# Kernel tuning notes

Measured on AMD Instinct MI355X. Metric: run time of the kernel, lower is better.

Reference implementation:

```python
import jax, jax.numpy as jnp
import numpy as np

THETA = 0.7
KS = 3          # deformable-conv kernel size
N = KS * KS     # 9 sampling points


def setup_inputs() -> dict:
    key = jax.random.key(0)
    k = jax.random.split(key, 7)
    B, C, H, W = 2, 256, 64, 64
    x = jax.random.normal(k[0], (B, C, H, W), jnp.float32)
    # offset-predicting conv (3x3, pad 1), 2*N output channels; small init so offsets are sane
    p_w = jax.random.normal(k[1], (2 * N, C, 3, 3), jnp.float32) * 0.01
    p_b = jax.random.normal(k[2], (2 * N,), jnp.float32) * 0.01
    # modulation conv (3x3, pad 1), N output channels
    m_w = jax.random.normal(k[3], (N, C, 3, 3), jnp.float32) * 0.01
    m_b = jnp.zeros((N,), jnp.float32)
    # final deform conv weight (applied as ks x ks, stride ks over the unfolded map), no bias
    dconv_w = jax.random.normal(k[4], (256, C, KS, KS), jnp.float32) * 0.05
    # central-difference conv raw weight, shape (Cout, Cin, 1, 5), no bias
    cdc_w = jax.random.normal(k[5], (256, C, 1, 5), jnp.float32) * 0.05
    return {"x": x, "p_w": p_w, "p_b": p_b, "m_w": m_w, "m_b": m_b,
            "dconv_w": dconv_w, "cdc_w": cdc_w}


def _conv2d(x, w, pad):
    return jax.lax.conv_general_dilated(
        x, w, window_strides=(1, 1), padding=pad,
        dimension_numbers=("NCHW", "OIHW", "NCHW"))


def deform_conv(x, p_w, p_b, m_w, m_b, dconv_w):
    B, C, H, W = x.shape
    same = [(1, 1), (1, 1)]
    offset = _conv2d(x, p_w, same) + p_b[None, :, None, None]          # [B,2N,H,W]
    m = jax.nn.sigmoid(_conv2d(x, m_w, same) + m_b[None, :, None, None])  # [B,N,H,W]

    xp = jnp.pad(x, ((0, 0), (0, 0), (1, 1), (1, 1)))  # zero padding 1
    Hp, Wp = H + 2, W + 2

    # p = p_0 + p_n + offset  (x = row coord, y = col coord; torch meshgrid 'ij')
    p_n_x = jnp.repeat(jnp.arange(-1, 2, dtype=x.dtype), 3)   # [-1,-1,-1,0,0,0,1,1,1]
    p_n_y = jnp.tile(jnp.arange(-1, 2, dtype=x.dtype), 3)     # [-1,0,1,-1,0,1,-1,0,1]
    rows = jnp.arange(1, H + 1, dtype=x.dtype)                # p_0_x
    cols = jnp.arange(1, W + 1, dtype=x.dtype)                # p_0_y
    px = offset[:, :N] + p_n_x[None, :, None, None] + rows[None, None, :, None]
    py = offset[:, N:] + p_n_y[None, :, None, None] + cols[None, None, None, :]
    px = jnp.transpose(px, (0, 2, 3, 1))  # [B,H,W,N]
    py = jnp.transpose(py, (0, 2, 3, 1))

    # integer corners from UNCLAMPED p (detached), as in the original
    fx = jnp.floor(jax.lax.stop_gradient(px))
    fy = jnp.floor(jax.lax.stop_gradient(py))
    qx0 = jnp.clip(fx, 0, Hp - 1)
    qy0 = jnp.clip(fy, 0, Wp - 1)
    qx1 = jnp.clip(fx + 1, 0, Hp - 1)
    qy1 = jnp.clip(fy + 1, 0, Wp - 1)

    # clamp p before computing bilinear weights (original order)
    pxc = jnp.clip(px, 0, Hp - 1)
    pyc = jnp.clip(py, 0, Wp - 1)
    g_lt = (1 + (qx0 - pxc)) * (1 + (qy0 - pyc))
    g_rb = (1 - (qx1 - pxc)) * (1 - (qy1 - pyc))
    g_lb = (1 + (qx0 - pxc)) * (1 - (qy1 - pyc))
    g_rt = (1 - (qx1 - pxc)) * (1 + (qy0 - pyc))

    xf = xp.reshape(B, C, Hp * Wp)

    def gather(qx, qy):
        idx = (qx.astype(jnp.int32) * Wp + qy.astype(jnp.int32)).reshape(B, 1, -1)
        return jnp.take_along_axis(xf, idx, axis=2).reshape(B, C, H, W, N)

    x_off = (g_lt[:, None] * gather(qx0, qy0)
             + g_rb[:, None] * gather(qx1, qy1)
             + g_lb[:, None] * gather(qx0, qy1)
             + g_rt[:, None] * gather(qx1, qy0))          # [B,C,H,W,N]
    x_off = x_off * jnp.transpose(m, (0, 2, 3, 1))[:, None]  # modulation broadcast over C

    # conv(ksxks, stride ks) over the unfolded map == contraction over the N taps;
    # tap n = 3r + c corresponds to kernel position (r, c)
    w = dconv_w.reshape(dconv_w.shape[0], C, N)
    return jnp.einsum("bchwn,ocn->bohw", x_off, w)


def cdc_conv(x, cdc_w):
    Co, Ci = cdc_w.shape[0], cdc_w.shape[1]
    z = jnp.zeros((Co, Ci, 1), cdc_w.dtype)
    wk = jnp.concatenate(
        [z, cdc_w[:, :, :, 0], z, cdc_w[:, :, :, 1], cdc_w[:, :, :, 2],
         cdc_w[:, :, :, 3], z, cdc_w[:, :, :, 4], z], axis=2
    ).reshape(Co, Ci, 3, 3)
    out_normal = _conv2d(x, wk, [(1, 1), (1, 1)])
    kdiff = cdc_w.sum(axis=(2, 3))[:, :, None, None]
    out_diff = _conv2d(x, kdiff, [(0, 0), (0, 0)])
    return out_normal - THETA * out_diff


def reference(x, p_w, p_b, m_w, m_b, dconv_w, cdc_w):
    out_dc = jax.nn.relu(deform_conv(x, p_w, p_b, m_w, m_b, dconv_w))
    out_cdc = jax.nn.relu(cdc_conv(x, cdc_w))
    return jnp.concatenate([out_dc, out_cdc], axis=1)  # [B,512,H,W]
```

## Files before the change

### kernel.cpp

```cpp
#include <hip/hip_runtime.h>
#include <hip/hip_bf16.h>
#include <math.h>

#define XT_BSTRIDE (66*66*256)
#define THETA_ 0.7f

typedef unsigned short u16;
typedef __attribute__((ext_vector_type(8))) short bf16x8;
typedef __attribute__((ext_vector_type(4))) float f32x4;

#define GLOAD16(gp, lp) __builtin_amdgcn_global_load_lds( \
    (const __attribute__((address_space(1))) unsigned int*)(gp), \
    (__attribute__((address_space(3))) unsigned int*)(lp), 16, 0, 0)

#define WAIT_VMCNT(N) asm volatile("s_waitcnt vmcnt(" #N ")" ::: "memory")

__device__ __forceinline__ void bar_fenced() {
  __builtin_amdgcn_sched_barrier(0);
  __builtin_amdgcn_s_barrier();
  __builtin_amdgcn_sched_barrier(0);
}

__device__ __forceinline__ float bf2f(u16 v) {
  union { unsigned u; float f; } x; x.u = ((unsigned)v) << 16; return x.f;
}
__device__ __forceinline__ u16 f2bf(float f) {
  __hip_bfloat16 h = __float2bfloat16(f);
  return *(u16*)&h;
}

__device__ __forceinline__ size_t swz_idx(int row, int k, int KT) {
  int kt = k >> 6, kc = (k >> 3) & 7, kj = k & 7;
  return (size_t)row * KT + kt * 64 + ((kc ^ (row & 7)) << 3) + kj;
}

__global__ __launch_bounds__(256) void prep(
    const float* __restrict__ x, const float* __restrict__ p_w,
    const float* __restrict__ m_w, const float* __restrict__ dconv_w,
    const float* __restrict__ cdc_w, u16* __restrict__ xTb,
    u16* __restrict__ W1t, u16* __restrict__ Wdt, u16* __restrict__ Wct) {
  int blk = blockIdx.x;
  if (blk < 512) {
    int cg = blk & 3;
    int h  = (blk >> 2) & 63;
    int b  = blk >> 8;
    __shared__ float tile[64][65];
    const float* xp = x + ((size_t)(b * 256 + cg * 64)) * 4096 + h * 64;
#pragma unroll
    for (int j = 0; j < 16; j++) {
      int idx = j * 256 + threadIdx.x;
      int ci = idx >> 6, w = idx & 63;
      tile[ci][w] = xp[(size_t)ci * 4096 + w];
    }
    __syncthreads();
    u16* xo = xTb + (size_t)b * XT_BSTRIDE + ((h + 1) * 66 + 1) * 256 + cg * 64;
#pragma unroll
    for (int j = 0; j < 16; j++) {
      int idx = j * 256 + threadIdx.x;
      int w = idx >> 6, ci = idx & 63;
      xo[(size_t)w * 256 + ci] = f2bf(tile[ci][w]);
    }
    return;
  }
  if (blk < 1032) {
    int i = (blk - 512) * 256 + threadIdx.x;
    if (i >= 133120) return;
    int c = i & 255;
    int j = i >> 8;
    int b = (j >= 260) ? 1 : 0;
    int r = j - b * 260;
    int hp, wp;
    if (r < 66)       { hp = 0;        wp = r; }
    else if (r < 132) { hp = 65;       wp = r - 66; }
    else if (r < 196) { hp = r - 131;  wp = 0; }
    else              { hp = r - 195;  wp = 65; }
    xTb[(size_t)b * XT_BSTRIDE + (hp * 66 + wp) * 256 + c] = 0;
    return;
  }
  int i = (blk - 1032) * 256 + threadIdx.x;
  if (i < 73728) {
    int o = i / 2304, k = i % 2304;
    int kp = k >> 8, c = k & 255;
    float v = 0.f;
    if (o < 18)      v = p_w[((size_t)o * 256 + c) * 9 + kp];
    else if (o < 27) v = m_w[((size_t)(o - 18) * 256 + c) * 9 + kp];
    W1t[swz_idx(o, k, 2304)] = f2bf(v);
    return;
  }
  int j = i - 73728;
  if (j < 589824) {
    int o = j / 2304, k = j % 2304;
    int n = k >> 8, c = k & 255;
    Wdt[swz_idx(o, k, 2304)] = f2bf(dconv_w[((size_t)o * 256 + c) * 9 + n]);
    return;
  }
  int j2 = j - 589824;
  if (j2 < 327680) {
    int o = j2 / 1280, k = j2 % 1280;
    int t = k >> 8, c = k & 255;
    const float* cw = cdc_w + ((size_t)o * 256 + c) * 5;
    float v = cw[t];
    if (t == 2) v -= THETA_ * (cw[0] + cw[1] + cw[2] + cw[3] + cw[4]);
    Wct[swz_idx(o, k, 1280)] = f2bf(v);
  }
}

__global__ __launch_bounds__(256) void gather_Ad(const u16* __restrict__ xTb,
                                                 const float* __restrict__ omp,
                                                 const float* __restrict__ p_b,
                                                 const float* __restrict__ m_b,
                                                 u16* __restrict__ Ad) {
  int gid = blockIdx.x * 256 + threadIdx.x;
  int q = gid & 31;
  int s = gid >> 5;
  int p = s / 9, n = s - p * 9;
  int b = p >> 12;
  int hw = p & 4095;
  int h = hw >> 6, w = hw & 63;

  float offx = p_b[n], offy = p_b[9 + n], mraw = m_b[n];
#pragma unroll
  for (int ks = 0; ks < 4; ks++) {
    const float* base = omp + ks * 221184 + b * 110592;
    offx += base[(size_t)n * 4096 + hw];
    offy += base[(size_t)(9 + n) * 4096 + hw];
    mraw += base[(size_t)(18 + n) * 4096 + hw];
  }
  float px = offx + (float)(h + n / 3);
  float py = offy + (float)(w + n % 3);
  float fx = floorf(px), fy = floorf(py);
  float qx0 = fminf(fmaxf(fx, 0.f), 65.f);
  float qy0 = fminf(fmaxf(fy, 0.f), 65.f);
  float qx1 = fminf(fmaxf(fx + 1.f, 0.f), 65.f);
  float qy1 = fminf(fmaxf(fy + 1.f, 0.f), 65.f);
  float pxc = fminf(fmaxf(px, 0.f), 65.f);
  float pyc = fminf(fmaxf(py, 0.f), 65.f);
  float gx0 = 1.f + (qx0 - pxc);
  float gx1 = 1.f - (qx1 - pxc);
  float gy0 = 1.f + (qy0 - pyc);
  float gy1 = 1.f - (qy1 - pyc);
  float m = 1.f / (1.f + expf(-mraw));
  int i0 = (int)qx0 * 66 + (int)qy0;
  int i1 = (int)qx1 * 66 + (int)qy1;
  int i2 = (int)qx0 * 66 + (int)qy1;
  int i3 = (int)qx1 * 66 + (int)qy0;
  float g0 = gx0 * gy0 * m, g1 = gx1 * gy1 * m;
  float g2 = gx0 * gy1 * m, g3 = gx1 * gy0 * m;

  const u16* xb = xTb + (size_t)b * XT_BSTRIDE + q * 8;
  bf16x8 a0 = *(const bf16x8*)(xb + (size_t)i0 * 256);
  bf16x8 a1 = *(const bf16x8*)(xb + (size_t)i1 * 256);
  bf16x8 a2 = *(const bf16x8*)(xb + (size_t)i2 * 256);
  bf16x8 a3 = *(const bf16x8*)(xb + (size_t)i3 * 256);
  bf16x8 ov;
#pragma unroll
  for (int j = 0; j < 8; j++) {
    float v = g0 * bf2f((u16)a0[j]) + g1 * bf2f((u16)a1[j]) +
              g2 * bf2f((u16)a2[j]) + g3 * bf2f((u16)a3[j]);
    ov[j] = (short)f2bf(v);
  }
  int k = n * 256 + q * 8;
  int kt = k >> 6, kc = (k >> 3) & 7;
  *(bf16x8*)(Ad + (size_t)p * 2304 + kt * 64 + (((kc ^ (p & 7)) << 3))) = ov;
}

template <int KTOT, int MODE>
__device__ __forceinline__ void gemm_body(
    const u16* __restrict__ Asrc, const u16* __restrict__ Bt,
    float* __restrict__ outp, int mt, int nt, u16* As, u16* Bs) {
  const int NKT = KTOT / 64;
  const int OCH0 = (MODE == 1) ? 256 : 0;
  int tid = threadIdx.x;
  int wid = tid >> 6, lane = tid & 63;
  int wr = wid >> 1, wc = wid & 1;
  int pbase = mt * 64;
  int obase = nt * 64;
  int l8 = lane >> 3, l7 = lane & 7;
  int lr = lane & 15, lg = lane >> 4;

  f32x4 acc[2][2];
#pragma unroll
  for (int i = 0; i < 2; i++)
#pragma unroll
    for (int j = 0; j < 2; j++) acc[i][j] = {0.f, 0.f, 0.f, 0.f};

  const int dh1[5] = {0, 1, 1, 1, 2}, dw1[5] = {1, 0, 1, 2, 1};

  auto stage = [&](int kt, u16* Ah, u16* Bh) {
    if (MODE == 0) {
#pragma unroll
      for (int i = 0; i < 2; i++) {
        int r0 = wid * 16 + i * 8;
        const u16* g = Asrc + (size_t)(pbase + r0 + l8) * KTOT + kt * 64 + (l7 << 3);
        GLOAD16(g, &Ah[r0 * 64]);
      }
    } else {
      int t = kt >> 2, c0 = (kt & 3) << 6;
      int dh = dh1[t], dw = dw1[t];
#pragma unroll
      for (int i = 0; i < 2; i++) {
        int r0 = wid * 16 + i * 8;
        int r = r0 + l8;
        int p = pbase + r;
        int b = p >> 12, hw = p & 4095, h = hw >> 6, w = hw & 63;
        int chunk = l7 ^ (r & 7);
        const u16* g = Asrc + (size_t)b * XT_BSTRIDE +
                       ((h + dh) * 66 + (w + dw)) * 256 + c0 + (chunk << 3);
        GLOAD16(g, &Ah[r0 * 64]);
      }
    }
#pragma unroll
    for (int i = 0; i < 2; i++) {
      int o0 = wid * 16 + i * 8;
      const u16* g = Bt + (size_t)(obase + o0 + l8) * KTOT + kt * 64 + (l7 << 3);
      GLOAD16(g, &Bh[o0 * 64]);
    }
  };

  stage(0, As, Bs);

  for (int it = 0; it < NKT; it++) {
    int cur = it & 1;
    u16* Ac = As + cur * 4096;
    u16* Bc = Bs + cur * 4096;

    bar_fenced();
    if (it + 1 < NKT) {
      stage(it + 1, As + (cur ^ 1) * 4096, Bs + (cur ^ 1) * 4096);
      WAIT_VMCNT(4);
    } else {
      WAIT_VMCNT(0);
    }
    bar_fenced();

    bf16x8 av[2][2], bv[2][2];
#pragma unroll
    for (int mf = 0; mf < 2; mf++) {
      int r = wr * 32 + mf * 16 + lr;
#pragma unroll
      for (int ks = 0; ks < 2; ks++) {
        int kc = ks * 4 + lg;
        av[mf][ks] = *(const bf16x8*)&Ac[r * 64 + ((kc ^ (r & 7)) << 3)];
      }
    }
#pragma unroll
    for (int nf = 0; nf < 2; nf++) {
      int o = wc * 32 + nf * 16 + lr;
#pragma unroll
      for (int ks = 0; ks < 2; ks++) {
        int kc = ks * 4 + lg;
        bv[nf][ks] = *(const bf16x8*)&Bc[o * 64 + ((kc ^ (o & 7)) << 3)];
      }
    }
#pragma unroll
    for (int nf = 0; nf < 2; nf++)
#pragma unroll
      for (int mf = 0; mf < 2; mf++)
#pragma unroll
        for (int ks = 0; ks < 2; ks++)
          acc[nf][mf] = __builtin_amdgcn_mfma_f32_16x16x32_bf16(
              bv[nf][ks], av[mf][ks], acc[nf][mf], 0, 0, 0);
  }

#pragma unroll
  for (int nf = 0; nf < 2; nf++)
#pragma unroll
    for (int mf = 0; mf < 2; mf++) {
      int p = pbase + wr * 32 + mf * 16 + lr;
      int hw = p & 4095, b = p >> 12;
      int og = OCH0 + obase + wc * 32 + nf * 16 + lg * 4;
      f32x4 v = acc[nf][mf];
#pragma unroll
      for (int e = 0; e < 4; e++)
        outp[(size_t)(b * 512 + og + e) * 4096 + hw] = fmaxf(v[e], 0.f);
    }
}

__device__ __forceinline__ void offmod_body(
    const u16* __restrict__ xTb, const u16* __restrict__ Bt,
    float* __restrict__ outp, int mt, int kt0, int nkt, u16* As, u16* Bs) {
  int tid = threadIdx.x;
  int wid = tid >> 6, lane = tid & 63;
  int pbase = mt * 128;
  int l8 = lane >> 3, l7 = lane & 7;
  int lr = lane & 15, lg = lane >> 4;

  f32x4 acc[2][2];
#pragma unroll
  for (int i = 0; i < 2; i++)
#pragma unroll
    for (int j = 0; j < 2; j++) acc[i][j] = {0.f, 0.f, 0.f, 0.f};

  auto stage = [&](int kt, u16* Ah, u16* Bh) {
    int t = kt >> 2, c0 = (kt & 3) << 6;
    int dh = t / 3, dw = t % 3;
#pragma unroll
    for (int i = 0; i < 4; i++) {
      int r0 = wid * 32 + i * 8;
      int r = r0 + l8;
      int p = pbase + r;
      int b = p >> 12, hw = p & 4095, h = hw >> 6, w = hw & 63;
      int chunk = l7 ^ (r & 7);
      const u16* g = xTb + (size_t)b * XT_BSTRIDE +
                     ((h + dh) * 66 + (w + dw)) * 256 + c0 + (chunk << 3);
      GLOAD16(g, &Ah[r0 * 64]);
    }
    {
      int o0 = wid * 8;
      const u16* g = Bt + (size_t)(o0 + l8) * 2304 + kt * 64 + (l7 << 3);
      GLOAD16(g, &Bh[o0 * 64]);
    }
  };

  stage(kt0, As, Bs);

  for (int it = 0; it < nkt; it++) {
    int cur = it & 1;
    u16* Ac = As + cur * 8192;
    u16* Bc = Bs + cur * 2048;

    bar_fenced();
    if (it + 1 < nkt) {
      stage(kt0 + it + 1, As + (cur ^ 1) * 8192, Bs + (cur ^ 1) * 2048);
      WAIT_VMCNT(5);
    } else {
      WAIT_VMCNT(0);
    }
    bar_fenced();

    bf16x8 av[2][2], bv[2][2];
#pragma unroll
    for (int mf = 0; mf < 2; mf++) {
      int r = wid * 32 + mf * 16 + lr;
#pragma unroll
      for (int ks = 0; ks < 2; ks++) {
        int kc = ks * 4 + lg;
        av[mf][ks] = *(const bf16x8*)&Ac[r * 64 + ((kc ^ (r & 7)) << 3)];
      }
    }
#pragma unroll
    for (int nf = 0; nf < 2; nf++) {
      int o = nf * 16 + lr;
#pragma unroll
      for (int ks = 0; ks < 2; ks++) {
        int kc = ks * 4 + lg;
        bv[nf][ks] = *(const bf16x8*)&Bc[o * 64 + ((kc ^ (o & 7)) << 3)];
      }
    }
#pragma unroll
    for (int nf = 0; nf < 2; nf++)
#pragma unroll
      for (int mf = 0; mf < 2; mf++)
#pragma unroll
        for (int ks = 0; ks < 2; ks++)
          acc[nf][mf] = __builtin_amdgcn_mfma_f32_16x16x32_bf16(
              bv[nf][ks], av[mf][ks], acc[nf][mf], 0, 0, 0);
  }

#pragma unroll
  for (int nf = 0; nf < 2; nf++)
#pragma unroll
    for (int mf = 0; mf < 2; mf++) {
      int p = pbase + wid * 32 + mf * 16 + lr;
      int hw = p & 4095, b = p >> 12;
      int o0 = nf * 16 + lg * 4;
      f32x4 v = acc[nf][mf];
#pragma unroll
      for (int e = 0; e < 4; e++) {
        int o = o0 + e;
        if (o < 27)
          outp[(size_t)(b * 27 + o) * 4096 + hw] = v[e];
      }
    }
}

__global__ __launch_bounds__(256) void gemm_offmod(const u16* __restrict__ xTb,
                                                   const u16* __restrict__ W1t,
                                                   float* __restrict__ omp) {
  __shared__ u16 As[2 * 128 * 64];
  __shared__ u16 Bs[2 * 32 * 64];
  int bid = blockIdx.x;
  int xcd = bid & 7;
  int i = bid >> 3;
  int mt = xcd * 8 + (i & 7);
  int ks = i >> 3;
  offmod_body(xTb, W1t, omp + ks * 221184, mt, ks * 9, 9, As, Bs);
}

__global__ __launch_bounds__(256, 4) void gemm_main(const u16* __restrict__ Ad,
                                                    const u16* __restrict__ xTb,
                                                    const u16* __restrict__ Wdt,
                                                    const u16* __restrict__ Wct,
                                                    float* __restrict__ out) {
  __shared__ u16 As[2 * 64 * 64];
  __shared__ u16 Bs[2 * 64 * 64];
  int bid = blockIdx.x;
  int fam = bid & 1;
  int idx = bid >> 1;
  int xcd = idx & 7;
  int j = idx >> 3;
  int mt = xcd * 16 + (j & 15);
  int nt = j >> 4;
  if (fam == 0) gemm_body<2304, 0>(Ad, Wdt, out, mt, nt, As, Bs);
  else          gemm_body<1280, 1>(xTb, Wct, out, mt, nt, As, Bs);
}

extern "C" void kernel_launch(void* const* d_in, const int* in_sizes, int n_in,
                              void* d_out, int out_size, void* d_ws, size_t ws_size,
                              hipStream_t stream) {
  (void)in_sizes; (void)n_in; (void)out_size; (void)ws_size;
  const float* x       = (const float*)d_in[0];
  const float* p_w     = (const float*)d_in[1];
  const float* p_b     = (const float*)d_in[2];
  const float* m_w     = (const float*)d_in[3];
  const float* m_b     = (const float*)d_in[4];
  const float* dconv_w = (const float*)d_in[5];
  const float* cdc_w   = (const float*)d_in[6];
  float* out = (float*)d_out;
  char* ws = (char*)d_ws;

  u16*   xTb  = (u16*)(ws);
  float* omp  = (float*)(ws + 4460544);
  u16*   W1t  = (u16*)(ws + 7999488);
  u16*   Wdt  = (u16*)(ws + 8146944);
  u16*   Wct  = (u16*)(ws + 9326592);
  u16*   Ad   = (u16*)(ws + 9981952);

  prep<<<4904, 256, 0, stream>>>(x, p_w, m_w, dconv_w, cdc_w, xTb, W1t, Wdt, Wct);
  gemm_offmod<<<256, 256, 0, stream>>>(xTb, W1t, omp);
  gather_Ad<<<9216, 256, 0, stream>>>(xTb, omp, p_b, m_b, Ad);
  gemm_main<<<1024, 256, 0, stream>>>(Ad, xTb, Wdt, Wct, out);
}
```

Before: 63.03 us.

## Pre-layout operands in MFMA fragment order and load directly to registers

Weights and the gathered deform matrix are now stored in MFMA fragment order, so each lane loads its bf16x8 operand straight from global memory without going through shared memory or barriers. gemm_main becomes a per-wave GEMM: each block covers 32 pixels and each wave 64 output channels, with register double-buffering across K tiles. This removes LDS staging and block synchronisation but gives up LDS reuse of A across waves, so global and L2 traffic rise. The CDC path loads shifted xTb rows directly with no swizzle.

```diff
diff --git a/kernel.cpp b/kernel.cpp
--- a/kernel.cpp
+++ b/kernel.cpp
@@ -32,6 +32,13 @@
 __device__ __forceinline__ size_t swz_idx(int row, int k, int KT) {
   int kt = k >> 6, kc = (k >> 3) & 7, kj = k & 7;
   return (size_t)row * KT + kt * 64 + ((kc ^ (row & 7)) << 3) + kj;
+}
+
+__device__ __forceinline__ size_t frag_idx(int row, int k, int NKT) {
+  int g = row >> 4;
+  int kt = k >> 6, ks = (k >> 5) & 1, lg = (k >> 3) & 3, j = k & 7;
+  int lane = (row & 15) + lg * 16;
+  return ((size_t)(g * NKT + kt) * 2 + ks) * 512 + lane * 8 + j;
 }
 
 __global__ __launch_bounds__(256) void prep(
@@ -91,7 +98,7 @@
   if (j < 589824) {
     int o = j / 2304, k = j % 2304;
     int n = k >> 8, c = k & 255;
-    Wdt[swz_idx(o, k, 2304)] = f2bf(dconv_w[((size_t)o * 256 + c) * 9 + n]);
+    Wdt[frag_idx(o, k, 36)] = f2bf(dconv_w[((size_t)o * 256 + c) * 9 + n]);
     return;
   }
   int j2 = j - 589824;
@@ -101,7 +108,7 @@
     const float* cw = cdc_w + ((size_t)o * 256 + c) * 5;
     float v = cw[t];
     if (t == 2) v -= THETA_ * (cw[0] + cw[1] + cw[2] + cw[3] + cw[4]);
-    Wct[swz_idx(o, k, 1280)] = f2bf(v);
+    Wct[frag_idx(o, k, 20)] = f2bf(v);
   }
 }
 
@@ -159,121 +166,111 @@
               g2 * bf2f((u16)a2[j]) + g3 * bf2f((u16)a3[j]);
     ov[j] = (short)f2bf(v);
   }
-  int k = n * 256 + q * 8;
-  int kt = k >> 6, kc = (k >> 3) & 7;
-  *(bf16x8*)(Ad + (size_t)p * 2304 + kt * 64 + (((kc ^ (p & 7)) << 3))) = ov;
-}
-
-template <int KTOT, int MODE>
-__device__ __forceinline__ void gemm_body(
-    const u16* __restrict__ Asrc, const u16* __restrict__ Bt,
-    float* __restrict__ outp, int mt, int nt, u16* As, u16* Bs) {
-  const int NKT = KTOT / 64;
+  int k0 = n * 256 + q * 8;
+  *(bf16x8*)(Ad + frag_idx(p, k0, 36)) = ov;
+}
+
+template <int NKT, int MODE>
+__device__ __forceinline__ void wave_gemm(
+    const u16* __restrict__ Af, const u16* __restrict__ xTb,
+    const u16* __restrict__ Bf, float* __restrict__ out, int wm, int wn) {
   const int OCH0 = (MODE == 1) ? 256 : 0;
-  int tid = threadIdx.x;
-  int wid = tid >> 6, lane = tid & 63;
-  int wr = wid >> 1, wc = wid & 1;
-  int pbase = mt * 64;
-  int obase = nt * 64;
-  int l8 = lane >> 3, l7 = lane & 7;
+  int lane = threadIdx.x & 63;
   int lr = lane & 15, lg = lane >> 4;
-
-  f32x4 acc[2][2];
-#pragma unroll
-  for (int i = 0; i < 2; i++)
+  int pbase = wm * 32;
+  int b = pbase >> 12;
+  const u16* xb = xTb + (size_t)b * XT_BSTRIDE;
+  const int dh1[5] = {0, 1, 1, 1, 2}, dw1[5] = {1, 0, 1, 2, 1};
+
+  f32x4 acc[4][2];
+#pragma unroll
+  for (int i = 0; i < 4; i++)
 #pragma unroll
     for (int j = 0; j < 2; j++) acc[i][j] = {0.f, 0.f, 0.f, 0.f};
 
-  const int dh1[5] = {0, 1, 1, 1, 2}, dw1[5] = {1, 0, 1, 2, 1};
-
-  auto stage = [&](int kt, u16* Ah, u16* Bh) {
+  int hA[2], wA[2];
+#pragma unroll
+  for (int mf = 0; mf < 2; mf++) {
+    int hw = (pbase + mf * 16 + lr) & 4095;
+    hA[mf] = hw >> 6; wA[mf] = hw & 63;
+  }
+
+  auto LOADA = [&](int kt, bf16x8 (&av)[2][2]) {
     if (MODE == 0) {
 #pragma unroll
-      for (int i = 0; i < 2; i++) {
-        int r0 = wid * 16 + i * 8;
-        const u16* g = Asrc + (size_t)(pbase + r0 + l8) * KTOT + kt * 64 + (l7 << 3);
-        GLOAD16(g, &Ah[r0 * 64]);
-      }
+      for (int mf = 0; mf < 2; mf++)
+#pragma unroll
+        for (int ks = 0; ks < 2; ks++)
+          av[mf][ks] = *(const bf16x8*)(Af +
+              ((size_t)((wm * 2 + mf) * NKT + kt) * 2 + ks) * 512 + lane * 8);
     } else {
-      int t = kt >> 2, c0 = (kt & 3) << 6;
-      int dh = dh1[t], dw = dw1[t];
-#pragma unroll
-      for (int i = 0; i < 2; i++) {
-        int r0 = wid * 16 + i * 8;
-        int r = r0 + l8;
-        int p = pbase + r;
-        int b = p >> 12, hw = p & 4095, h = hw >> 6, w = hw & 63;
-        int chunk = l7 ^ (r & 7);
-        const u16* g = Asrc + (size_t)b * XT_BSTRIDE +
-                       ((h + dh) * 66 + (w + dw)) * 256 + c0 + (chunk << 3);
-        GLOAD16(g, &Ah[r0 * 64]);
-      }
-    }
-#pragma unroll
-    for (int i = 0; i < 2; i++) {
-      int o0 = wid * 16 + i * 8;
-      const u16* g = Bt + (size_t)(obase + o0 + l8) * KTOT + kt * 64 + (l7 << 3);
-      GLOAD16(g, &Bh[o0 * 64]);
+#pragma unroll
+      for (int mf = 0; mf < 2; mf++)
+#pragma unroll
+        for (int ks = 0; ks < 2; ks++) {
+          int k = kt * 64 + ks * 32 + lg * 8;
+          int t = k >> 8, c = k & 255;
+          av[mf][ks] = *(const bf16x8*)(xb +
+              ((hA[mf] + dh1[t]) * 66 + (wA[mf] + dw1[t])) * 256 + c);
+        }
     }
   };
-
-  stage(0, As, Bs);
-
-  for (int it = 0; it < NKT; it++) {
-    int cur = it & 1;
-    u16* Ac = As + cur * 4096;
-    u16* Bc = Bs + cur * 4096;
-
-    bar_fenced();
-    if (it + 1 < NKT) {
-      stage(it + 1, As + (cur ^ 1) * 4096, Bs + (cur ^ 1) * 4096);
-      WAIT_VMCNT(4);
-    } else {
-      WAIT_VMCNT(0);
-    }
-    bar_fenced();
-
-    bf16x8 av[2][2], bv[2][2];
-#pragma unroll
-    for (int mf = 0; mf < 2; mf++) {
-      int r = wr * 32 + mf * 16 + lr;
-#pragma unroll
-      for (int ks = 0; ks < 2; ks++) {
-        int kc = ks * 4 + lg;
-        av[mf][ks] = *(const bf16x8*)&Ac[r * 64 + ((kc ^ (r & 7)) << 3)];
-      }
-    }
-#pragma unroll
-    for (int nf = 0; nf < 2; nf++) {
-      int o = wc * 32 + nf * 16 + lr;
-#pragma unroll
-      for (int ks = 0; ks < 2; ks++) {
-        int kc = ks * 4 + lg;
-        bv[nf][ks] = *(const bf16x8*)&Bc[o * 64 + ((kc ^ (o & 7)) << 3)];
-      }
-    }
-#pragma unroll
-    for (int nf = 0; nf < 2; nf++)
+  auto LOADB = [&](int kt, bf16x8 (&bv)[4][2]) {
+#pragma unroll
+    for (int nf = 0; nf < 4; nf++)
+#pragma unroll
+      for (int ks = 0; ks < 2; ks++)
+        bv[nf][ks] = *(const bf16x8*)(Bf +
+            ((size_t)((wn * 4 + nf) * NKT + kt) * 2 + ks) * 512 + lane * 8);
+  };
+  auto MFMA = [&](bf16x8 (&av)[2][2], bf16x8 (&bv)[4][2]) {
+#pragma unroll
+    for (int nf = 0; nf < 4; nf++)
 #pragma unroll
       for (int mf = 0; mf < 2; mf++)
 #pragma unroll
         for (int ks = 0; ks < 2; ks++)
           acc[nf][mf] = __builtin_amdgcn_mfma_f32_16x16x32_bf16(
               bv[nf][ks], av[mf][ks], acc[nf][mf], 0, 0, 0);
-  }
-
-#pragma unroll
-  for (int nf = 0; nf < 2; nf++)
+  };
+
+  bf16x8 aE[2][2], bE[4][2], aO[2][2], bO[4][2];
+  LOADA(0, aE); LOADB(0, bE);
+  for (int kt = 0; kt < NKT; kt += 2) {
+    LOADA(kt + 1, aO); LOADB(kt + 1, bO);
+    MFMA(aE, bE);
+    if (kt + 2 < NKT) { LOADA(kt + 2, aE); LOADB(kt + 2, bE); }
+    MFMA(aO, bO);
+  }
+
+#pragma unroll
+  for (int nf = 0; nf < 4; nf++)
 #pragma unroll
     for (int mf = 0; mf < 2; mf++) {
-      int p = pbase + wr * 32 + mf * 16 + lr;
-      int hw = p & 4095, b = p >> 12;
-      int og = OCH0 + obase + wc * 32 + nf * 16 + lg * 4;
+      int p = pbase + mf * 16 + lr;
+      int hw = p & 4095;
+      int og = OCH0 + wn * 64 + nf * 16 + lg * 4;
       f32x4 v = acc[nf][mf];
 #pragma unroll
       for (int e = 0; e < 4; e++)
-        outp[(size_t)(b * 512 + og + e) * 4096 + hw] = fmaxf(v[e], 0.f);
-    }
+        out[(size_t)(b * 512 + og + e) * 4096 + hw] = fmaxf(v[e], 0.f);
+    }
+}
+
+__global__ __launch_bounds__(256) void gemm_main(const u16* __restrict__ Ad,
+                                                 const u16* __restrict__ xTb,
+                                                 const u16* __restrict__ Wdt,
+                                                 const u16* __restrict__ Wct,
+                                                 float* __restrict__ out) {
+  int bid = blockIdx.x;
+  int fam = bid & 1;
+  int idx = bid >> 1;
+  int xcd = idx & 7;
+  int j = idx >> 3;
+  int wm = xcd * 32 + j;
+  int wn = threadIdx.x >> 6;
+  if (fam == 0) wave_gemm<36, 0>(Ad, xTb, Wdt, out, wm, wn);
+  else          wave_gemm<20, 1>(Ad, xTb, Wct, out, wm, wn);
 }
 
 __device__ __forceinline__ void offmod_body(
@@ -385,24 +382,6 @@
   int mt = xcd * 8 + (i & 7);
   int ks = i >> 3;
   offmod_body(xTb, W1t, omp + ks * 221184, mt, ks * 9, 9, As, Bs);
-}
-
-__global__ __launch_bounds__(256, 4) void gemm_main(const u16* __restrict__ Ad,
-                                                    const u16* __restrict__ xTb,
-                                                    const u16* __restrict__ Wdt,
-                                                    const u16* __restrict__ Wct,
-                                                    float* __restrict__ out) {
-  __shared__ u16 As[2 * 64 * 64];
-  __shared__ u16 Bs[2 * 64 * 64];
-  int bid = blockIdx.x;
-  int fam = bid & 1;
-  int idx = bid >> 1;
-  int xcd = idx & 7;
-  int j = idx >> 3;
-  int mt = xcd * 16 + (j & 15);
-  int nt = j >> 4;
-  if (fam == 0) gemm_body<2304, 0>(Ad, Wdt, out, mt, nt, As, Bs);
-  else          gemm_body<1280, 1>(xTb, Wct, out, mt, nt, As, Bs);
 }
 
 extern "C" void kernel_launch(void* const* d_in, const int* in_sizes, int n_in,
@@ -429,5 +408,5 @@
   prep<<<4904, 256, 0, stream>>>(x, p_w, m_w, dconv_w, cdc_w, xTb, W1t, Wdt, Wct);
   gemm_offmod<<<256, 256, 0, stream>>>(xTb, W1t, omp);
   gather_Ad<<<9216, 256, 0, stream>>>(xTb, omp, p_b, m_b, Ad);
-  gemm_main<<<1024, 256, 0, stream>>>(Ad, xTb, Wdt, Wct, out);
-}
+  gemm_main<<<512, 256, 0, stream>>>(Ad, xTb, Wdt, Wct, out);
+}
```

After: 92.47 us. 46.7% more time.
